# Kernel optimization log

Measured on AMD Instinct MI355X. Metric: run time of the kernel, lower is better.

## Reference

```python
import jax, jax.numpy as jnp
import numpy as np

NQ = 16               # num_qubits
S = 1 << NQ           # 65536 superposition states
D = 128               # quantum_dim
B = 4                 # batch
ENT = 0.8             # entanglement_strength
DECO_T = 100.0        # decoherence_time


def setup_inputs() -> dict:
    key = jax.random.key(0)
    ks = jax.random.split(key, 7)
    return {
        "input_features": jax.random.normal(ks[0], (B, D), jnp.float32),
        # complex quantum_weights, stored as separate real/imag parts
        "qw_re": jax.random.normal(ks[1], (S, D), jnp.float32),
        "qw_im": jax.random.normal(ks[2], (S, D), jnp.float32),
        "rotation_angles": jax.random.normal(ks[3], (NQ, 3), jnp.float32),
        "entanglement_matrix": jax.random.normal(ks[4], (NQ, NQ), jnp.float32),
        # per-qubit measurement Linear(D, D): y = x @ W_i.T + b_i
        "meas_W": jax.random.normal(ks[5], (NQ, D, D), jnp.float32) / np.sqrt(D).astype(np.float32),
        "meas_b": jax.random.normal(ks[6], (NQ, D), jnp.float32) * np.float32(0.01),
    }


def reference(input_features, qw_re, qw_im, rotation_angles, entanglement_matrix, meas_W, meas_b):
    b = input_features.shape[0]  # input is only consulted for batch size (as in the original)
    qw = qw_re + 1j * qw_im                              # [S, D] complex64
    # ---- apply_quantum_gates: cumulative per-qubit phase = exp(i * sum of all angles)
    phase = jnp.exp(1j * rotation_angles.sum())
    state = jnp.broadcast_to((qw * phase)[None], (b, S, D))  # [B, S, D]
    # entanglement: softmax(16x16) mixes across a qubit-factored view of the state dim
    ew = jax.nn.softmax(entanglement_matrix, axis=-1).astype(state.dtype)  # [NQ, NQ]
    ent = jnp.einsum('qp,bpkd->bqkd', ew, state.reshape(b, NQ, S // NQ, D)).reshape(b, S, D)
    state = ENT * ent + (1.0 - ENT) * state
    # ---- simulate_decoherence (timer = 1 on first call)
    coh = jnp.exp(jnp.float32(-1.0 / DECO_T))
    kn = jax.random.split(jax.random.key(1), 3)
    inv_sqrt2 = np.float32(1.0 / np.sqrt(2.0))
    noise = (jax.random.normal(kn[0], (b, S, D)) + 1j * jax.random.normal(kn[1], (b, S, D))) \
            * (inv_sqrt2 * (1.0 - coh) * np.float32(0.1))
    state = state * coh + noise
    # ---- quantum_measurement: one categorical draw over S states per (batch, column)
    # multinomial(p[:, j], 1) == Gumbel-max over log p; normalization constant cancels.
    logits = jnp.log(jnp.real(state) ** 2 + jnp.imag(state) ** 2 + 1e-20)  # log |amp|^2, [B,S,D]
    u = jax.random.uniform(kn[2], (b, S, D), minval=1e-7, maxval=1.0)
    idx = jnp.argmax(logits - jnp.log(-jnp.log(u)), axis=1)  # [B, D] sampled state index
    # one-hot collapsed state; only rows 0..NQ-1 are consumed by the measurement ops,
    # so we avoid materializing the full [B, S, D] one-hot.
    measured = (idx[:, None, :] == jnp.arange(NQ)[None, :, None]).astype(jnp.float32)  # [B, NQ, D]
    outs = jnp.einsum('bnd,ned->bne', measured, meas_W) + meas_b[None]  # per-qubit Linear
    return outs.mean(axis=1)  # [B, D]
```

## Files before the change

kernel.cpp:

```cpp
#include <hip/hip_runtime.h>
#include <stdint.h>
#include <math.h>

constexpr int D_ = 128;
constexpr int KDIM = 4096;
constexpr uint32_t NTH = 4096u * 128u;

#define DELTA   0.00385f
#define RELM    1.0002f
#define WLO_PAD 1e-3f
#define EPS_CMP 1e-3f

__host__ __device__ static inline void tfround(uint32_t& x0, uint32_t& x1, int r) {
    x0 += x1;
    x1 = (x1 << r) | (x1 >> (32 - r));
    x1 ^= x0;
}

__host__ __device__ static inline void tf2x32(uint32_t k0, uint32_t k1,
                                              uint32_t x0, uint32_t x1,
                                              uint32_t& o0, uint32_t& o1) {
    uint32_t ks2 = k0 ^ k1 ^ 0x1BD11BDAu;
    x0 += k0; x1 += k1;
    tfround(x0, x1, 13); tfround(x0, x1, 15); tfround(x0, x1, 26); tfround(x0, x1, 6);
    x0 += k1;  x1 += ks2 + 1u;
    tfround(x0, x1, 17); tfround(x0, x1, 29); tfround(x0, x1, 16); tfround(x0, x1, 24);
    x0 += ks2; x1 += k0 + 2u;
    tfround(x0, x1, 13); tfround(x0, x1, 15); tfround(x0, x1, 26); tfround(x0, x1, 6);
    x0 += k0;  x1 += k1 + 3u;
    tfround(x0, x1, 17); tfround(x0, x1, 29); tfround(x0, x1, 16); tfround(x0, x1, 24);
    x0 += k1;  x1 += ks2 + 4u;
    tfround(x0, x1, 13); tfround(x0, x1, 15); tfround(x0, x1, 26); tfround(x0, x1, 6);
    x0 += ks2; x1 += k0 + 5u;
    o0 = x0; o1 = x1;
}

__device__ __forceinline__ float neglog_hybrid(float u, float nz) {
    float p4 = fmaf(nz, 0.2f, 0.25f);
    float p3 = fmaf(nz, p4, 0.33333334f);
    float p2 = fmaf(nz, p3, 0.5f);
    float poly = fmaf(nz, p2, 1.0f);
    float ts = nz * poly;
    float tl = -__logf(u);
    return (nz < 0.01f) ? ts : tl;
}

__device__ __forceinline__ float erfinv_fast(float x) {
    float w = -__logf(fmaf(-x, x, 1.0f));
    float p;
    if (w < 5.0f) {
        w -= 2.5f;
        p = 2.81022636e-08f;
        p = fmaf(p, w, 3.43273939e-07f);
        p = fmaf(p, w, -3.5233877e-06f);
        p = fmaf(p, w, -4.39150654e-06f);
        p = fmaf(p, w, 0.00021858087f);
        p = fmaf(p, w, -0.00125372503f);
        p = fmaf(p, w, -0.00417768164f);
        p = fmaf(p, w, 0.246640727f);
        p = fmaf(p, w, 1.50140941f);
    } else {
        float wt = -__logf((1.0f - x) * (1.0f + x));
        float v = sqrtf(wt) - 3.0f;
        p = -0.000200214257f;
        p = fmaf(p, v, 0.000100950558f);
        p = fmaf(p, v, 0.00134934322f);
        p = fmaf(p, v, -0.00367342844f);
        p = fmaf(p, v, 0.00573950773f);
        p = fmaf(p, v, -0.0076224613f);
        p = fmaf(p, v, 0.00943887047f);
        p = fmaf(p, v, 1.00167406f);
        p = fmaf(p, v, 2.83297682f);
    }
    return p * x;
}

__device__ __forceinline__ uint32_t ordmap(float x) {
    uint32_t u = __float_as_uint(x);
    return (u & 0x80000000u) ? ~u : (u | 0x80000000u);
}
__device__ __forceinline__ float ordunmap(uint32_t m) {
    uint32_t u = (m & 0x80000000u) ? (m & 0x7FFFFFFFu) : ~m;
    return __uint_as_float(u);
}

__global__ __launch_bounds__(512) void qsl_prep(const float* __restrict__ ang,
                                                const float* __restrict__ ent,
                                                float* __restrict__ ws_f,
                                                unsigned long long* __restrict__ keys,
                                                uint32_t* __restrict__ Mlo,
                                                float coh) {
    __shared__ float sm[16][16];
    int t = threadIdx.x;
    keys[t] = 0ULL;
    if (t < 512) Mlo[t] = 0u;
    if (t < 16) {
        float row[16];
        float m = -INFINITY;
        for (int j = 0; j < 16; j++) { row[j] = ent[t * 16 + j]; m = fmaxf(m, row[j]); }
        float s = 0.f;
        for (int j = 0; j < 16; j++) { row[j] = expf(row[j] - m); s += row[j]; }
        float inv = 1.0f / s;
        for (int j = 0; j < 16; j++) sm[t][j] = row[j] * inv;
    }
    if (t == 0) {
        float a = 0.f;
        for (int i = 0; i < 48; i++) a += ang[i];
        ws_f[256] = cosf(a);
        ws_f[257] = sinf(a);
    }
    __syncthreads();
    if (t < 256) {
        int q = t >> 4, p = t & 15;
        float c = (0.8f * coh) * sm[q][p];
        if (q == p) c += 0.2f * coh;
        ws_f[t] = c;
    }
}

__global__ __launch_bounds__(256) void qsl_bound(const float* __restrict__ qre,
                                                 const float* __restrict__ qim,
                                                 const float* __restrict__ Cg,
                                                 uint32_t* __restrict__ Mlo,
                                                 unsigned long long* __restrict__ maskArr,
                                                 float* __restrict__ whiArr,
                                                 uint32_t kC0, uint32_t kC1) {
    const int d = threadIdx.x;
    const int y = threadIdx.y;
    const int kk = blockIdx.x * 2 + y;
    const uint32_t g = (uint32_t)kk * 128u + (uint32_t)d;

    const float pr = Cg[256], pi = Cg[257];

    float eLo[16], eHi[16];
    {
        float vr[16], vi[16];
#pragma unroll
        for (int p = 0; p < 16; p++) {
            int off = (p * KDIM + kk) * D_ + d;
            float ar = qre[off], ai = qim[off];
            vr[p] = fmaf(pr, ar, -(pi * ai));
            vi[p] = fmaf(pi, ar, pr * ai);
        }
#pragma unroll
        for (int q = 0; q < 16; q++) {
            float br = 0.f, bi = 0.f;
#pragma unroll
            for (int p = 0; p < 16; p++) {
                float c = Cg[q * 16 + p];
                br = fmaf(c, vr[p], br);
                bi = fmaf(c, vi[p], bi);
            }
            float abr = fabsf(br), abi = fabsf(bi);
            float hr = abr + DELTA, hq = abi + DELTA;
            float Phi_hi = fmaf(hr, hr, fmaf(hq, hq, 1e-20f));
            float lr = fmaxf(abr - DELTA, 0.f), lq = fmaxf(abi - DELTA, 0.f);
            float Phi_lo = fmaf(lr, lr, fmaf(lq, lq, 1e-20f));
            eLo[q] = __builtin_amdgcn_rcpf(Phi_lo);
            eHi[q] = __builtin_amdgcn_rcpf(Phi_hi);
        }
    }

    unsigned long long mask64 = 0ull;
    float whi[4];

#pragma unroll 1
    for (int b = 0; b < 4; b++) {
        const uint32_t nb = g + ((uint32_t)b << 23);
        float ph[16];
        float mlo_t = INFINITY, mhi_t = INFINITY;
#pragma unroll
        for (int q = 0; q < 16; q++) {
            uint32_t w0, w1;
            tf2x32(kC0, kC1, 0u, nb + ((uint32_t)q << 19), w0, w1);
            uint32_t r = w0 ^ w1;
            float f = __uint_as_float((r >> 9) | 0x3f800000u) - 1.0f;
            float nz = 1.0f - f;
            float t = neglog_hybrid(f, nz);
            float plo = t * eLo[q];
            float phi_ = t * eHi[q];
            ph[q] = phi_;
            mlo_t = fminf(mlo_t, plo);
            mhi_t = fminf(mhi_t, phi_);
        }
        uint32_t mloc = 0u;
        float thr = mlo_t * RELM;
#pragma unroll
        for (int q = 0; q < 16; q++)
            if (ph[q] <= thr) mloc |= (1u << q);
        mask64 |= ((unsigned long long)mloc) << (b * 16);

        float wlo = -__logf(mlo_t) - WLO_PAD;
        whi[b]    = -__logf(mhi_t);
        uint32_t mu = ordmap(wlo);
        uint32_t cur = Mlo[b * 128 + d];
        if (mu > cur) atomicMax(&Mlo[b * 128 + d], mu);
    }

    maskArr[g] = mask64;
#pragma unroll
    for (int b = 0; b < 4; b++) whiArr[b * NTH + g] = whi[b];
}

__global__ __launch_bounds__(256) void qsl_resolve(const float* __restrict__ qre,
                                                   const float* __restrict__ qim,
                                                   const float* __restrict__ Cg,
                                                   const uint32_t* __restrict__ Mlo,
                                                   const unsigned long long* __restrict__ maskArr,
                                                   const float* __restrict__ whiArr,
                                                   unsigned long long* __restrict__ keys,
                                                   uint32_t kA0, uint32_t kA1,
                                                   uint32_t kB0, uint32_t kB1,
                                                   uint32_t kC0, uint32_t kC1,
                                                   float nc) {
    const int d = threadIdx.x;
    const int y = threadIdx.y;
    const int kk = blockIdx.x * 2 + y;
    const uint32_t g = (uint32_t)kk * 128u + (uint32_t)d;

    unsigned long long mask64 = maskArr[g];
    unsigned long long live = 0ull;
#pragma unroll
    for (int b = 0; b < 4; b++) {
        float whi = whiArr[b * NTH + g];
        float mref = ordunmap(Mlo[b * 128 + d]);
        if (!(whi < mref - EPS_CMP)) live |= 0xFFFFull << (b * 16);
    }
    mask64 &= live;
    if (mask64 == 0ull) return;

    const float pr = Cg[256], pi = Cg[257];
    float vr[16], vi[16];
#pragma unroll
    for (int p = 0; p < 16; p++) {
        int off = (p * KDIM + kk) * D_ + d;
        float ar = qre[off], ai = qim[off];
        vr[p] = fmaf(pr, ar, -(pi * ai));
        vi[p] = fmaf(pi, ar, pr * ai);
    }

    const float ULO = 1e-7f;
    const float UDF = 1.0f - 1e-7f;
    const float NLO = -0.99999994f;
    const float NDF = 1.0f - NLO;

    while (mask64) {
        int bit = __ffsll(mask64) - 1;
        mask64 &= mask64 - 1ull;
        uint32_t q = (uint32_t)bit & 15u;
        int b = bit >> 4;
        uint32_t n = g + ((uint32_t)bit << 19);

        float br = 0.f, bi = 0.f;
        const float4* C4 = reinterpret_cast<const float4*>(Cg + (q << 4));
#pragma unroll
        for (int j = 0; j < 4; j++) {
            float4 c = C4[j];
            br = fmaf(c.x, vr[j*4+0], br); bi = fmaf(c.x, vi[j*4+0], bi);
            br = fmaf(c.y, vr[j*4+1], br); bi = fmaf(c.y, vi[j*4+1], bi);
            br = fmaf(c.z, vr[j*4+2], br); bi = fmaf(c.z, vi[j*4+2], bi);
            br = fmaf(c.w, vr[j*4+3], br); bi = fmaf(c.w, vi[j*4+3], bi);
        }

        uint32_t w0, w1;
        tf2x32(kC0, kC1, 0u, n, w0, w1);
        uint32_t rC = w0 ^ w1;
        tf2x32(kA0, kA1, 0u, n, w0, w1);
        uint32_t rA = w0 ^ w1;
        tf2x32(kB0, kB1, 0u, n, w0, w1);
        uint32_t rB = w0 ^ w1;

        float fu = __uint_as_float((rC >> 9) | 0x3f800000u) - 1.0f;
        float u  = __fadd_rn(__fmul_rn(fu, UDF), ULO);
        float f0 = __uint_as_float((rA >> 9) | 0x3f800000u) - 1.0f;
        float x0 = __fadd_rn(__fmul_rn(f0, NDF), NLO);
        float f1 = __uint_as_float((rB >> 9) | 0x3f800000u) - 1.0f;
        float x1 = __fadd_rn(__fmul_rn(f1, NDF), NLO);
        float nr = 1.41421356f * erfinv_fast(x0);
        float ni = 1.41421356f * erfinv_fast(x1);
        float ar = fmaf(nc, nr, br);
        float ai = fmaf(nc, ni, bi);
        float logit = __logf(fmaf(ar, ar, fmaf(ai, ai, 1e-20f)));
        float nz = 1.0f - u;
        float t = neglog_hybrid(u, nz);
        float gv = __logf(t);
        float v = logit - gv;

        uint32_t s = (q << 12) + (uint32_t)kk;
        uint32_t mu = ordmap(v);
        unsigned long long kp =
            ((unsigned long long)mu << 32) |
            (unsigned long long)(0xFFFFFFFFu - s);
        atomicMax(&keys[b * 128 + d], kp);
    }
}

__global__ __launch_bounds__(128) void qsl_out(const unsigned long long* __restrict__ keys,
                                               const float* __restrict__ mW,
                                               const float* __restrict__ mb,
                                               float* __restrict__ out) {
    int b = blockIdx.x, e = threadIdx.x;
    __shared__ uint32_t idx_s[128];
    unsigned long long kp = keys[b * 128 + e];
    idx_s[e] = 0xFFFFFFFFu - (uint32_t)(kp & 0xFFFFFFFFull);
    __syncthreads();

    float acc = 0.f;
#pragma unroll
    for (int n = 0; n < 16; n++) acc += mb[n * 128 + e];
    for (int dd = 0; dd < 128; dd++) {
        uint32_t m = idx_s[dd];
        if (m < 16u) acc += mW[(m * 128 + e) * 128 + dd];
    }
    out[b * 128 + e] = acc * 0.0625f;
}

extern "C" void kernel_launch(void* const* d_in, const int* in_sizes, int n_in,
                              void* d_out, int out_size, void* d_ws, size_t ws_size,
                              hipStream_t stream) {
    (void)in_sizes; (void)n_in; (void)out_size; (void)ws_size;
    const float* qre = (const float*)d_in[1];
    const float* qim = (const float*)d_in[2];
    const float* ang = (const float*)d_in[3];
    const float* ent = (const float*)d_in[4];
    const float* mW  = (const float*)d_in[5];
    const float* mb  = (const float*)d_in[6];
    float* out = (float*)d_out;

    char* ws = (char*)d_ws;
    float* ws_f = (float*)ws;
    unsigned long long* keys = (unsigned long long*)(ws + 4096);
    uint32_t* Mlo = (uint32_t*)(ws + 8192);
    unsigned long long* maskArr = (unsigned long long*)(ws + 12288);
    float* whiArr = (float*)(ws + 12288 + (size_t)NTH * 8);

    uint32_t kn[6];
    tf2x32(0u, 1u, 0u, 0u, kn[0], kn[1]);
    tf2x32(0u, 1u, 0u, 1u, kn[2], kn[3]);
    tf2x32(0u, 1u, 0u, 2u, kn[4], kn[5]);

    float coh = expf(-0.01f);
    float nc  = (0.70710678f * (1.0f - coh)) * 0.1f;

    hipLaunchKernelGGL(qsl_prep, dim3(1), dim3(512), 0, stream, ang, ent, ws_f, keys, Mlo, coh);
    hipLaunchKernelGGL(qsl_bound, dim3(2048), dim3(128, 2), 0, stream,
                       qre, qim, ws_f, Mlo, maskArr, whiArr, kn[4], kn[5]);
    hipLaunchKernelGGL(qsl_resolve, dim3(2048), dim3(128, 2), 0, stream,
                       qre, qim, ws_f, Mlo, maskArr, whiArr, keys,
                       kn[0], kn[1], kn[2], kn[3], kn[4], kn[5], nc);
    hipLaunchKernelGGL(qsl_out, dim3(4), dim3(128), 0, stream, keys, mW, mb, out);
}
```

Baseline: 114.9 us.

## Seed lower bound from subset, sweep with threshold test, compact candidates into list

```diff
diff --git a/kernel.cpp b/kernel.cpp
--- a/kernel.cpp
+++ b/kernel.cpp
@@ -4,12 +4,12 @@
 
 constexpr int D_ = 128;
 constexpr int KDIM = 4096;
-constexpr uint32_t NTH = 4096u * 128u;
+constexpr uint32_t CAP = 262144u;
 
 #define DELTA   0.00385f
-#define RELM    1.0002f
 #define WLO_PAD 1e-3f
-#define EPS_CMP 1e-3f
+#define EPS_T   0.002f
+#define MARG    1.001f
 
 __host__ __device__ static inline void tfround(uint32_t& x0, uint32_t& x1, int r) {
     x0 += x1;
@@ -89,11 +89,13 @@
                                                 float* __restrict__ ws_f,
                                                 unsigned long long* __restrict__ keys,
                                                 uint32_t* __restrict__ Mlo,
+                                                uint32_t* __restrict__ cnt,
                                                 float coh) {
     __shared__ float sm[16][16];
     int t = threadIdx.x;
     keys[t] = 0ULL;
-    if (t < 512) Mlo[t] = 0u;
+    Mlo[t] = 0u;
+    if (t == 0) cnt[0] = 0u;
     if (t < 16) {
         float row[16];
         float m = -INFINITY;
@@ -118,21 +120,85 @@
     }
 }
 
-__global__ __launch_bounds__(256) void qsl_bound(const float* __restrict__ qre,
+__global__ __launch_bounds__(256) void qsl_seed(const float* __restrict__ qre,
+                                                const float* __restrict__ qim,
+                                                const float* __restrict__ Cg,
+                                                uint32_t* __restrict__ Mlo,
+                                                uint32_t kC0, uint32_t kC1) {
+    const int d = threadIdx.x;
+    const int y = threadIdx.y;
+    const int kk = blockIdx.x * 2 + y;
+    const uint32_t g = (uint32_t)kk * 128u + (uint32_t)d;
+
+    const float pr = Cg[256], pi = Cg[257];
+
+    float eLo[16];
+    {
+        float vr[16], vi[16];
+#pragma unroll
+        for (int p = 0; p < 16; p++) {
+            int off = (p * KDIM + kk) * D_ + d;
+            float ar = qre[off], ai = qim[off];
+            vr[p] = fmaf(pr, ar, -(pi * ai));
+            vi[p] = fmaf(pi, ar, pr * ai);
+        }
+#pragma unroll
+        for (int q = 0; q < 16; q++) {
+            float br = 0.f, bi = 0.f;
+#pragma unroll
+            for (int p = 0; p < 16; p++) {
+                float c = Cg[q * 16 + p];
+                br = fmaf(c, vr[p], br);
+                bi = fmaf(c, vi[p], bi);
+            }
+            float abr = fabsf(br), abi = fabsf(bi);
+            float lr = fmaxf(abr - DELTA, 0.f), lq = fmaxf(abi - DELTA, 0.f);
+            float Phi_lo = fmaf(lr, lr, fmaf(lq, lq, 1e-20f));
+            eLo[q] = __builtin_amdgcn_rcpf(Phi_lo);
+        }
+    }
+
+#pragma unroll 1
+    for (int b = 0; b < 4; b++) {
+        const uint32_t nb = g + ((uint32_t)b << 23);
+        float mlo_t = INFINITY;
+#pragma unroll
+        for (int q = 0; q < 16; q++) {
+            uint32_t w0, w1;
+            tf2x32(kC0, kC1, 0u, nb + ((uint32_t)q << 19), w0, w1);
+            uint32_t r = w0 ^ w1;
+            float f = __uint_as_float((r >> 9) | 0x3f800000u) - 1.0f;
+            float nz = 1.0f - f;
+            float t = neglog_hybrid(f, nz);
+            mlo_t = fminf(mlo_t, t * eLo[q]);
+        }
+        float wlo = -__logf(mlo_t) - WLO_PAD;
+        uint32_t mu = ordmap(wlo);
+        uint32_t cur = Mlo[b * 128 + d];
+        if (mu > cur) atomicMax(&Mlo[b * 128 + d], mu);
+    }
+}
+
+__global__ __launch_bounds__(256) void qsl_sweep(const float* __restrict__ qre,
                                                  const float* __restrict__ qim,
                                                  const float* __restrict__ Cg,
-                                                 uint32_t* __restrict__ Mlo,
-                                                 unsigned long long* __restrict__ maskArr,
-                                                 float* __restrict__ whiArr,
+                                                 const uint32_t* __restrict__ Mlo,
+                                                 uint32_t* __restrict__ cnt,
+                                                 uint4* __restrict__ list,
                                                  uint32_t kC0, uint32_t kC1) {
     const int d = threadIdx.x;
     const int y = threadIdx.y;
     const int kk = blockIdx.x * 2 + y;
     const uint32_t g = (uint32_t)kk * 128u + (uint32_t)d;
 
+    float E0 = __expf(EPS_T - ordunmap(Mlo[0 * 128 + d]));
+    float E1 = __expf(EPS_T - ordunmap(Mlo[1 * 128 + d]));
+    float E2 = __expf(EPS_T - ordunmap(Mlo[2 * 128 + d]));
+    float E3 = __expf(EPS_T - ordunmap(Mlo[3 * 128 + d]));
+
     const float pr = Cg[256], pi = Cg[257];
 
-    float eLo[16], eHi[16];
+    float PhM[16];
     {
         float vr[16], vi[16];
 #pragma unroll
@@ -154,144 +220,125 @@
             float abr = fabsf(br), abi = fabsf(bi);
             float hr = abr + DELTA, hq = abi + DELTA;
             float Phi_hi = fmaf(hr, hr, fmaf(hq, hq, 1e-20f));
-            float lr = fmaxf(abr - DELTA, 0.f), lq = fmaxf(abi - DELTA, 0.f);
-            float Phi_lo = fmaf(lr, lr, fmaf(lq, lq, 1e-20f));
-            eLo[q] = __builtin_amdgcn_rcpf(Phi_lo);
-            eHi[q] = __builtin_amdgcn_rcpf(Phi_hi);
+            PhM[q] = Phi_hi * MARG;
         }
     }
 
     unsigned long long mask64 = 0ull;
-    float whi[4];
 
 #pragma unroll 1
     for (int b = 0; b < 4; b++) {
         const uint32_t nb = g + ((uint32_t)b << 23);
-        float ph[16];
-        float mlo_t = INFINITY, mhi_t = INFINITY;
+        float Eb = (b == 0) ? E0 : ((b == 1) ? E1 : ((b == 2) ? E2 : E3));
+        float ft[16];
+#pragma unroll
+        for (int q = 0; q < 16; q++) ft[q] = fmaf(-PhM[q], Eb, 0.99999976f);
+
+        uint32_t mloc = 0u;
 #pragma unroll
         for (int q = 0; q < 16; q++) {
             uint32_t w0, w1;
             tf2x32(kC0, kC1, 0u, nb + ((uint32_t)q << 19), w0, w1);
             uint32_t r = w0 ^ w1;
             float f = __uint_as_float((r >> 9) | 0x3f800000u) - 1.0f;
-            float nz = 1.0f - f;
-            float t = neglog_hybrid(f, nz);
-            float plo = t * eLo[q];
-            float phi_ = t * eHi[q];
-            ph[q] = phi_;
-            mlo_t = fminf(mlo_t, plo);
-            mhi_t = fminf(mhi_t, phi_);
-        }
-        uint32_t mloc = 0u;
-        float thr = mlo_t * RELM;
-#pragma unroll
-        for (int q = 0; q < 16; q++)
-            if (ph[q] <= thr) mloc |= (1u << q);
+            if (f >= ft[q]) mloc |= (1u << q);
+        }
         mask64 |= ((unsigned long long)mloc) << (b * 16);
-
-        float wlo = -__logf(mlo_t) - WLO_PAD;
-        whi[b]    = -__logf(mhi_t);
-        uint32_t mu = ordmap(wlo);
-        uint32_t cur = Mlo[b * 128 + d];
-        if (mu > cur) atomicMax(&Mlo[b * 128 + d], mu);
-    }
-
-    maskArr[g] = mask64;
-#pragma unroll
-    for (int b = 0; b < 4; b++) whiArr[b * NTH + g] = whi[b];
+    }
+
+    if (mask64 != 0ull) {
+        uint32_t idx = atomicAdd(cnt, 1u);
+        if (idx < CAP)
+            list[idx] = make_uint4(g, (uint32_t)mask64, (uint32_t)(mask64 >> 32), 0u);
+    }
 }
 
 __global__ __launch_bounds__(256) void qsl_resolve(const float* __restrict__ qre,
                                                    const float* __restrict__ qim,
                                                    const float* __restrict__ Cg,
-                                                   const uint32_t* __restrict__ Mlo,
-                                                   const unsigned long long* __restrict__ maskArr,
-                                                   const float* __restrict__ whiArr,
+                                                   const uint32_t* __restrict__ cnt,
+                                                   const uint4* __restrict__ list,
                                                    unsigned long long* __restrict__ keys,
                                                    uint32_t kA0, uint32_t kA1,
                                                    uint32_t kB0, uint32_t kB1,
                                                    uint32_t kC0, uint32_t kC1,
                                                    float nc) {
-    const int d = threadIdx.x;
-    const int y = threadIdx.y;
-    const int kk = blockIdx.x * 2 + y;
-    const uint32_t g = (uint32_t)kk * 128u + (uint32_t)d;
-
-    unsigned long long mask64 = maskArr[g];
-    unsigned long long live = 0ull;
-#pragma unroll
-    for (int b = 0; b < 4; b++) {
-        float whi = whiArr[b * NTH + g];
-        float mref = ordunmap(Mlo[b * 128 + d]);
-        if (!(whi < mref - EPS_CMP)) live |= 0xFFFFull << (b * 16);
-    }
-    mask64 &= live;
-    if (mask64 == 0ull) return;
-
+    uint32_t n_items = cnt[0];
+    if (n_items > CAP) n_items = CAP;
+    const uint32_t stride = gridDim.x * blockDim.x;
     const float pr = Cg[256], pi = Cg[257];
-    float vr[16], vi[16];
-#pragma unroll
-    for (int p = 0; p < 16; p++) {
-        int off = (p * KDIM + kk) * D_ + d;
-        float ar = qre[off], ai = qim[off];
-        vr[p] = fmaf(pr, ar, -(pi * ai));
-        vi[p] = fmaf(pi, ar, pr * ai);
-    }
 
     const float ULO = 1e-7f;
     const float UDF = 1.0f - 1e-7f;
     const float NLO = -0.99999994f;
     const float NDF = 1.0f - NLO;
 
-    while (mask64) {
-        int bit = __ffsll(mask64) - 1;
-        mask64 &= mask64 - 1ull;
-        uint32_t q = (uint32_t)bit & 15u;
-        int b = bit >> 4;
-        uint32_t n = g + ((uint32_t)bit << 19);
-
-        float br = 0.f, bi = 0.f;
-        const float4* C4 = reinterpret_cast<const float4*>(Cg + (q << 4));
-#pragma unroll
-        for (int j = 0; j < 4; j++) {
-            float4 c = C4[j];
-            br = fmaf(c.x, vr[j*4+0], br); bi = fmaf(c.x, vi[j*4+0], bi);
-            br = fmaf(c.y, vr[j*4+1], br); bi = fmaf(c.y, vi[j*4+1], bi);
-            br = fmaf(c.z, vr[j*4+2], br); bi = fmaf(c.z, vi[j*4+2], bi);
-            br = fmaf(c.w, vr[j*4+3], br); bi = fmaf(c.w, vi[j*4+3], bi);
-        }
-
-        uint32_t w0, w1;
-        tf2x32(kC0, kC1, 0u, n, w0, w1);
-        uint32_t rC = w0 ^ w1;
-        tf2x32(kA0, kA1, 0u, n, w0, w1);
-        uint32_t rA = w0 ^ w1;
-        tf2x32(kB0, kB1, 0u, n, w0, w1);
-        uint32_t rB = w0 ^ w1;
-
-        float fu = __uint_as_float((rC >> 9) | 0x3f800000u) - 1.0f;
-        float u  = __fadd_rn(__fmul_rn(fu, UDF), ULO);
-        float f0 = __uint_as_float((rA >> 9) | 0x3f800000u) - 1.0f;
-        float x0 = __fadd_rn(__fmul_rn(f0, NDF), NLO);
-        float f1 = __uint_as_float((rB >> 9) | 0x3f800000u) - 1.0f;
-        float x1 = __fadd_rn(__fmul_rn(f1, NDF), NLO);
-        float nr = 1.41421356f * erfinv_fast(x0);
-        float ni = 1.41421356f * erfinv_fast(x1);
-        float ar = fmaf(nc, nr, br);
-        float ai = fmaf(nc, ni, bi);
-        float logit = __logf(fmaf(ar, ar, fmaf(ai, ai, 1e-20f)));
-        float nz = 1.0f - u;
-        float t = neglog_hybrid(u, nz);
-        float gv = __logf(t);
-        float v = logit - gv;
-
-        uint32_t s = (q << 12) + (uint32_t)kk;
-        uint32_t mu = ordmap(v);
-        unsigned long long kp =
-            ((unsigned long long)mu << 32) |
-            (unsigned long long)(0xFFFFFFFFu - s);
-        atomicMax(&keys[b * 128 + d], kp);
+    for (uint32_t i = blockIdx.x * blockDim.x + threadIdx.x; i < n_items; i += stride) {
+        uint4 e = list[i];
+        const uint32_t g = e.x;
+        unsigned long long mask64 =
+            ((unsigned long long)e.z << 32) | (unsigned long long)e.y;
+        const int kk = (int)(g >> 7);
+        const int d = (int)(g & 127u);
+
+        float vr[16], vi[16];
+#pragma unroll
+        for (int p = 0; p < 16; p++) {
+            int off = (p * KDIM + kk) * D_ + d;
+            float ar = qre[off], ai = qim[off];
+            vr[p] = fmaf(pr, ar, -(pi * ai));
+            vi[p] = fmaf(pi, ar, pr * ai);
+        }
+
+        while (mask64) {
+            int bit = __ffsll(mask64) - 1;
+            mask64 &= mask64 - 1ull;
+            uint32_t q = (uint32_t)bit & 15u;
+            int b = bit >> 4;
+            uint32_t n = g + ((uint32_t)bit << 19);
+
+            float br = 0.f, bi = 0.f;
+            const float4* C4 = reinterpret_cast<const float4*>(Cg + (q << 4));
+#pragma unroll
+            for (int j = 0; j < 4; j++) {
+                float4 c = C4[j];
+                br = fmaf(c.x, vr[j*4+0], br); bi = fmaf(c.x, vi[j*4+0], bi);
+                br = fmaf(c.y, vr[j*4+1], br); bi = fmaf(c.y, vi[j*4+1], bi);
+                br = fmaf(c.z, vr[j*4+2], br); bi = fmaf(c.z, vi[j*4+2], bi);
+                br = fmaf(c.w, vr[j*4+3], br); bi = fmaf(c.w, vi[j*4+3], bi);
+            }
+
+            uint32_t w0, w1;
+            tf2x32(kC0, kC1, 0u, n, w0, w1);
+            uint32_t rC = w0 ^ w1;
+            tf2x32(kA0, kA1, 0u, n, w0, w1);
+            uint32_t rA = w0 ^ w1;
+            tf2x32(kB0, kB1, 0u, n, w0, w1);
+            uint32_t rB = w0 ^ w1;
+
+            float fu = __uint_as_float((rC >> 9) | 0x3f800000u) - 1.0f;
+            float u  = __fadd_rn(__fmul_rn(fu, UDF), ULO);
+            float f0 = __uint_as_float((rA >> 9) | 0x3f800000u) - 1.0f;
+            float x0 = __fadd_rn(__fmul_rn(f0, NDF), NLO);
+            float f1 = __uint_as_float((rB >> 9) | 0x3f800000u) - 1.0f;
+            float x1 = __fadd_rn(__fmul_rn(f1, NDF), NLO);
+            float nr = 1.41421356f * erfinv_fast(x0);
+            float ni = 1.41421356f * erfinv_fast(x1);
+            float ar = fmaf(nc, nr, br);
+            float ai = fmaf(nc, ni, bi);
+            float logit = __logf(fmaf(ar, ar, fmaf(ai, ai, 1e-20f)));
+            float nz = 1.0f - u;
+            float t = neglog_hybrid(u, nz);
+            float gv = __logf(t);
+            float v = logit - gv;
+
+            uint32_t s = (q << 12) + (uint32_t)kk;
+            uint32_t mu = ordmap(v);
+            unsigned long long kp =
+                ((unsigned long long)mu << 32) |
+                (unsigned long long)(0xFFFFFFFFu - s);
+            atomicMax(&keys[b * 128 + d], kp);
+        }
     }
 }
 
@@ -331,8 +378,8 @@
     float* ws_f = (float*)ws;
     unsigned long long* keys = (unsigned long long*)(ws + 4096);
     uint32_t* Mlo = (uint32_t*)(ws + 8192);
-    unsigned long long* maskArr = (unsigned long long*)(ws + 12288);
-    float* whiArr = (float*)(ws + 12288 + (size_t)NTH * 8);
+    uint32_t* cnt = (uint32_t*)(ws + 10240);
+    uint4* list  = (uint4*)(ws + 12288);
 
     uint32_t kn[6];
     tf2x32(0u, 1u, 0u, 0u, kn[0], kn[1]);
@@ -342,11 +389,14 @@
     float coh = expf(-0.01f);
     float nc  = (0.70710678f * (1.0f - coh)) * 0.1f;
 
-    hipLaunchKernelGGL(qsl_prep, dim3(1), dim3(512), 0, stream, ang, ent, ws_f, keys, Mlo, coh);
-    hipLaunchKernelGGL(qsl_bound, dim3(2048), dim3(128, 2), 0, stream,
-                       qre, qim, ws_f, Mlo, maskArr, whiArr, kn[4], kn[5]);
-    hipLaunchKernelGGL(qsl_resolve, dim3(2048), dim3(128, 2), 0, stream,
-                       qre, qim, ws_f, Mlo, maskArr, whiArr, keys,
+    hipLaunchKernelGGL(qsl_prep, dim3(1), dim3(512), 0, stream,
+                       ang, ent, ws_f, keys, Mlo, cnt, coh);
+    hipLaunchKernelGGL(qsl_seed, dim3(128), dim3(128, 2), 0, stream,
+                       qre, qim, ws_f, Mlo, kn[4], kn[5]);
+    hipLaunchKernelGGL(qsl_sweep, dim3(2048), dim3(128, 2), 0, stream,
+                       qre, qim, ws_f, Mlo, cnt, list, kn[4], kn[5]);
+    hipLaunchKernelGGL(qsl_resolve, dim3(256), dim3(256), 0, stream,
+                       qre, qim, ws_f, cnt, list, keys,
                        kn[0], kn[1], kn[2], kn[3], kn[4], kn[5], nc);
     hipLaunchKernelGGL(qsl_out, dim3(4), dim3(128), 0, stream, keys, mW, mb, out);
 }
```

After: 127.5 us. 11.0% more time.
